# Kernel tuning notes

Measured on AMD Instinct MI355X. Metric: run time of the kernel, lower is better.

## Reference

```python
import jax, jax.numpy as jnp
import numpy as np
from jax import lax

B, D, H, W = 16, 256, 64, 64
P = 8  # patchsize
EPS = 1e-5


def setup_inputs() -> dict:
    key = jax.random.key(0)
    ks = jax.random.split(key, 8)
    s = 0.02
    return {
        "x": jax.random.normal(ks[0], (B, D, H, W), jnp.float32),
        "wq": jax.random.normal(ks[1], (D, D), jnp.float32) * s,
        "bq": jnp.zeros((D,), jnp.float32),
        "wk": jax.random.normal(ks[2], (D, D), jnp.float32) * s,
        "bk": jnp.zeros((D,), jnp.float32),
        "wv": jax.random.normal(ks[3], (D, D), jnp.float32) * s,
        "bv": jnp.zeros((D,), jnp.float32),
        "w_out": jax.random.normal(ks[4], (D, D, 3, 3), jnp.float32) * s,
        "b_out": jnp.zeros((D,), jnp.float32),
        "gamma": jnp.ones((D,), jnp.float32),
        "beta": jnp.zeros((D,), jnp.float32),
        "bn_mean": jnp.zeros((D,), jnp.float32),
        "bn_var": jnp.ones((D,), jnp.float32),
    }


def _conv1x1(x, w, b):
    # x: [b,c,h,w], w: [o,c] (1x1 conv) -> [b,o,h,w]
    return jnp.einsum('bchw,oc->bohw', x, w) + b[None, :, None, None]


def _to_patches(t, p):
    # [b,d,h,w] -> [b, p*p, d*hh*ww]  (matches view+permute(0,2,4,1,3,5)+view)
    b, d, h, w = t.shape
    hh, ww = h // p, w // p
    t = t.reshape(b, d, p, hh, p, ww).transpose(0, 2, 4, 1, 3, 5)
    return t.reshape(b, p * p, d * hh * ww)


def reference(x, wq, bq, wk, bk, wv, bv, w_out, b_out, gamma, beta, bn_mean, bn_var):
    b, d, h, w = x.shape
    p = P
    hh, ww = h // p, w // p

    q = _to_patches(_conv1x1(x, wq, bq), p)  # [b, p^2, d*hh*ww]
    k = _to_patches(_conv1x1(x, wk, bk), p)
    v = _to_patches(_conv1x1(x, wv, bv), p)

    scale = 1.0 / jnp.sqrt(jnp.asarray(q.shape[-1], q.dtype))
    scores = jnp.einsum('bqe,bke->bqk', q, k) * scale  # [b, p^2, p^2]
    attn = jax.nn.softmax(scores, axis=-1)
    out = jnp.einsum('bqk,bke->bqe', attn, v)  # [b, p^2, d*hh*ww]

    # [b,p,p,d,hh,ww] -> permute(0,3,1,4,2,5) -> [b,d,h,w]
    out = out.reshape(b, p, p, d, hh, ww).transpose(0, 3, 1, 4, 2, 5).reshape(b, d, h, w)

    # 3x3 conv, padding 1
    y = lax.conv_general_dilated(out, w_out, window_strides=(1, 1),
                                 padding=((1, 1), (1, 1)),
                                 dimension_numbers=('NCHW', 'OIHW', 'NCHW'))
    y = y + b_out[None, :, None, None]

    # BatchNorm2d (eval mode with running stats)
    inv = gamma / jnp.sqrt(bn_var + EPS)
    y = (y - bn_mean[None, :, None, None]) * inv[None, :, None, None] + beta[None, :, None, None]

    # LeakyReLU(0.2)
    return jnp.where(y >= 0, y, 0.2 * y)
```

## Files before the change

kernel.cpp:

```cpp
#include <hip/hip_runtime.h>
#include <hip/hip_bf16.h>

#define BB 16
#define SS 4096

typedef __attribute__((ext_vector_type(8))) short short8;
typedef __attribute__((ext_vector_type(4))) float float4v;

__global__ __launch_bounds__(256) void wprep_qkv(
    const float* __restrict__ wq, const float* __restrict__ wk,
    const float* __restrict__ wv, __hip_bfloat16* __restrict__ blob) {
  int chunk = blockIdx.x * 256 + threadIdx.x;
  int lane = chunk & 63;
  int ob = (chunk >> 6) & 15;
  int cb = (chunk >> 10) & 7;
  int which = chunk >> 13;
  const float* W = (which == 0) ? wq : (which == 1) ? wk : wv;
  int o = ob * 16 + (lane & 15);
  int c0 = cb * 32 + (lane >> 4) * 8;
  const float* p = W + o * 256 + c0;
  union { uint4 u; __hip_bfloat16 h[8]; } t;
#pragma unroll
  for (int j = 0; j < 8; ++j) t.h[j] = __float2bfloat16(p[j]);
  *reinterpret_cast<uint4*>(blob + (size_t)chunk * 8) = t.u;
}

__global__ __launch_bounds__(256) void qkv_mfma(
    const float* __restrict__ x, const __hip_bfloat16* __restrict__ blob,
    const float* __restrict__ bq, const float* __restrict__ bk,
    const float* __restrict__ bv,
    __hip_bfloat16* __restrict__ qb, __hip_bfloat16* __restrict__ kb,
    __hip_bfloat16* __restrict__ vb) {
  __shared__ short ls[64 * 40];
  const int which = blockIdx.z;
  const int b = blockIdx.y;
  const int s0 = blockIdx.x * 64;
  const float* bias = (which == 0) ? bq : (which == 1) ? bk : bv;
  __hip_bfloat16* outb = (which == 0) ? qb : kb;
  const int tid = threadIdx.x;
  const int wave = tid >> 6, lane = tid & 63;
  const int q = lane >> 4, m = lane & 15;
  const int sl = tid & 63;
  const int cg = tid >> 6;
  float4v acc[4][4] = {};

  for (int cb = 0; cb < 8; ++cb) {
    __syncthreads();
    {
      const float* xp = x + ((size_t)(b * 256 + cb * 32 + cg * 8)) * SS + s0 + sl;
      union { uint4 u; __hip_bfloat16 h[8]; } t;
#pragma unroll
      for (int i = 0; i < 8; ++i)
        t.h[i] = __float2bfloat16(xp[(size_t)i * SS]);
      *reinterpret_cast<uint4*>(&ls[sl * 40 + cg * 8]) = t.u;
    }
    __syncthreads();
    short8 af[4];
#pragma unroll
    for (int of = 0; of < 4; ++of)
      af[of] = *reinterpret_cast<const short8*>(
          blob +
          ((size_t)(((which * 8 + cb) * 16 + wave * 4 + of) * 64 + lane)) * 8);
    short8 xf[4];
#pragma unroll
    for (int sf = 0; sf < 4; ++sf)
      xf[sf] = *reinterpret_cast<const short8*>(&ls[(sf * 16 + m) * 40 + q * 8]);
#pragma unroll
    for (int of = 0; of < 4; ++of)
#pragma unroll
      for (int sf = 0; sf < 4; ++sf)
        acc[of][sf] = __builtin_amdgcn_mfma_f32_16x16x32_bf16(
            af[of], xf[sf], acc[of][sf], 0, 0, 0);
  }
  if (which == 2) {
    const int h = s0 >> 6;
#pragma unroll
    for (int of = 0; of < 4; ++of) {
      int o_base = wave * 64 + of * 16 + q * 4;
#pragma unroll
      for (int sf = 0; sf < 4; ++sf) {
        int w = sf * 16 + m;
        union { uint2 u; __hip_bfloat16 hh[4]; } t;
#pragma unroll
        for (int r = 0; r < 4; ++r)
          t.hh[r] = __float2bfloat16(acc[of][sf][r] + bias[o_base + r]);
        *reinterpret_cast<uint2*>(
            vb + ((size_t)((b * 64 + h) * 64 + w)) * 256 + o_base) = t.u;
      }
    }
  } else {
#pragma unroll
    for (int of = 0; of < 4; ++of) {
      int o_base = wave * 64 + of * 16 + q * 4;
#pragma unroll
      for (int r = 0; r < 4; ++r) {
        int o = o_base + r;
        float bi = bias[o];
        __hip_bfloat16* op = outb + ((size_t)(b * 256 + o)) * SS + s0 + m;
#pragma unroll
        for (int sf = 0; sf < 4; ++sf)
          op[sf * 16] = __float2bfloat16(acc[of][sf][r] + bi);
      }
    }
  }
}

__global__ __launch_bounds__(256) void scores_mfma(
    const __hip_bfloat16* __restrict__ qb, const __hip_bfloat16* __restrict__ kb,
    float* __restrict__ scores) {
  const int b = blockIdx.y;
  const int d0 = blockIdx.x * 16;
  const int tid = threadIdx.x;
  const int wave = tid >> 6, lane = tid & 63;
  const int q = lane >> 4, m = lane & 15;
  const int t = wave * 16 + m;
  const int arow = (t >> 3) * 8;
  const int acol = (t & 7) * 8;
  float4v acc[4] = {};

  for (int dd = 0; dd < 16; ++dd) {
    const int d = d0 + dd;
    const __hip_bfloat16* qp = qb + ((size_t)(b * 256 + d)) * SS;
    const __hip_bfloat16* kp = kb + ((size_t)(b * 256 + d)) * SS;
#pragma unroll
    for (int khalf = 0; khalf < 2; ++khalf) {
      const int oh = khalf * 4 + q;
      short8 af = *reinterpret_cast<const short8*>(
          qp + (arow + oh) * 64 + acol);
      short8 bf[4];
#pragma unroll
      for (int nt = 0; nt < 4; ++nt) {
        int tp = nt * 16 + m;
        bf[nt] = *reinterpret_cast<const short8*>(
            kp + ((tp >> 3) * 8 + oh) * 64 + (tp & 7) * 8);
      }
#pragma unroll
      for (int nt = 0; nt < 4; ++nt)
        acc[nt] = __builtin_amdgcn_mfma_f32_16x16x32_bf16(af, bf[nt], acc[nt],
                                                          0, 0, 0);
    }
  }
#pragma unroll
  for (int nt = 0; nt < 4; ++nt)
#pragma unroll
    for (int r = 0; r < 4; ++r)
      atomicAdd(&scores[(b * 64 + wave * 16 + q * 4 + r) * 64 + nt * 16 + m],
                acc[nt][r]);
}

__global__ __launch_bounds__(64) void softmax_kernel(
    const float* __restrict__ scores, __hip_bfloat16* __restrict__ attnb) {
  const int t = blockIdx.x;
  const int b = blockIdx.y;
  const int lane = threadIdx.x;
  float v = scores[(b * 64 + t) * 64 + lane] * 0.0078125f;
  float m = v;
#pragma unroll
  for (int off = 32; off >= 1; off >>= 1) m = fmaxf(m, __shfl_xor(m, off));
  float e = __expf(v - m);
  float s = e;
#pragma unroll
  for (int off = 32; off >= 1; off >>= 1) s += __shfl_xor(s, off);
  attnb[(b * 64 + t) * 64 + lane] = __float2bfloat16(e / s);
}

__global__ __launch_bounds__(256) void apply_mfma(
    const __hip_bfloat16* __restrict__ attnb, const __hip_bfloat16* __restrict__ vb,
    __hip_bfloat16* __restrict__ zb) {
  __shared__ short Vs[64][268];
  const int off = blockIdx.x;
  const int b = blockIdx.y;
  const int oh = off >> 3, ow = off & 7;
  const int tid = threadIdx.x;
#pragma unroll
  for (int i = 0; i < 8; ++i) {
    int chunk = i * 256 + tid;
    int tp = chunk >> 5;
    int cg = chunk & 31;
    int hh = (tp >> 3) * 8 + oh;
    int wwp = (tp & 7) * 8 + ow;
    uint4 val = *reinterpret_cast<const uint4*>(
        vb + ((size_t)((b * 64 + hh) * 64 + wwp)) * 256 + cg * 8);
    *reinterpret_cast<uint4*>(&Vs[tp][cg * 8]) = val;
  }
  __syncthreads();
  const int wave = tid >> 6, lane = tid & 63;
  const int q = lane >> 4, m = lane & 15;
  float4v acc[4][4] = {};
#pragma unroll
  for (int ks = 0; ks < 2; ++ks) {
    short8 af[4];
#pragma unroll
    for (int mt = 0; mt < 4; ++mt)
      af[mt] = *reinterpret_cast<const short8*>(
          attnb + (b * 64 + mt * 16 + m) * 64 + ks * 32 + q * 8);
    short8 bf[4];
#pragma unroll
    for (int nt = 0; nt < 4; ++nt) {
      int d = wave * 64 + nt * 16 + m;
      union { short8 v; short s[8]; } t;
#pragma unroll
      for (int j = 0; j < 8; ++j) t.s[j] = Vs[ks * 32 + q * 8 + j][d];
      bf[nt] = t.v;
    }
#pragma unroll
    for (int mt = 0; mt < 4; ++mt)
#pragma unroll
      for (int nt = 0; nt < 4; ++nt)
        acc[mt][nt] = __builtin_amdgcn_mfma_f32_16x16x32_bf16(
            af[mt], bf[nt], acc[mt][nt], 0, 0, 0);
  }
#pragma unroll
  for (int mt = 0; mt < 4; ++mt)
#pragma unroll
    for (int r = 0; r < 4; ++r) {
      int t = mt * 16 + q * 4 + r;
      int h = (t >> 3) * 8 + oh;
      int w = (t & 7) * 8 + ow;
      __hip_bfloat16* base = zb + ((size_t)((b * 64 + h) * 64 + w)) * 256;
#pragma unroll
      for (int nt = 0; nt < 4; ++nt)
        base[wave * 64 + nt * 16 + m] = __float2bfloat16(acc[mt][nt][r]);
    }
}

__global__ __launch_bounds__(256) void wprep(
    const float* __restrict__ wo, __hip_bfloat16* __restrict__ blob) {
  int chunk = blockIdx.x * 256 + threadIdx.x;
  int l = chunk & 63;
  int ob = (chunk >> 6) & 15;
  int cb = (chunk >> 10) & 7;
  int tap = chunk >> 13;
  int o = ob * 16 + (l & 15);
  int c0 = cb * 32 + (l >> 4) * 8;
  union { uint4 u; __hip_bfloat16 h[8]; } t;
#pragma unroll
  for (int j = 0; j < 8; ++j)
    t.h[j] = __float2bfloat16(wo[((size_t)(o * 256 + c0 + j)) * 9 + tap]);
  *reinterpret_cast<uint4*>(blob + (size_t)chunk * 8) = t.u;
}

__global__ __launch_bounds__(256) void conv_mfma(
    const __hip_bfloat16* __restrict__ z, const __hip_bfloat16* __restrict__ blob,
    const float* __restrict__ bo, const float* __restrict__ gm,
    const float* __restrict__ bt, const float* __restrict__ mn,
    const float* __restrict__ vr, float* __restrict__ out) {
  __shared__ short zs[2][3 * 66 * 40];
  const int idx0 = blockIdx.x;
  const int h = (idx0 & 7) * 8 + ((idx0 >> 3) & 7);
  const int b = idx0 >> 6;
  const int tid = threadIdx.x;
  const int wave = tid >> 6, lane = tid & 63;
  const int q = lane >> 4, m = lane & 15;
  float4v acc[4][4] = {};

  int s_r[4], s_wp[4], s_cg[4];
  bool s_ok[4];
  const __hip_bfloat16* s_base[4];
#pragma unroll
  for (int k = 0; k < 4; ++k) {
    int idx = tid + k * 256;
    bool act = idx < 792;
    int cg = idx & 3;
    int t2 = idx >> 2;
    int wpos = act ? (t2 % 66) : 0;
    int r = act ? (t2 / 66) : 0;
    int h_in = h - 1 + r;
    int w_in = wpos - 1;
    bool ok = act && h_in >= 0 && h_in < 64 && w_in >= 0 && w_in < 64;
    s_r[k] = r; s_wp[k] = wpos; s_cg[k] = cg; s_ok[k] = ok && act;
    s_ok[k] = ok;
    s_base[k] = z + ((size_t)((b * 64 + h_in) * 64 + w_in)) * 256 + cg * 8;
    if (!act) s_ok[k] = false;
    if (idx >= 792) { s_r[k] = 0; s_wp[k] = 0; s_cg[k] = 0; }
  }
  bool s_act[4];
#pragma unroll
  for (int k = 0; k < 4; ++k) s_act[k] = (tid + k * 256) < 792;

  uint4 pf[4];
#pragma unroll
  for (int k = 0; k < 4; ++k)
    pf[k] = s_ok[k] ? *reinterpret_cast<const uint4*>(s_base[k])
                    : make_uint4(0u, 0u, 0u, 0u);
#pragma unroll
  for (int k = 0; k < 4; ++k)
    if (s_act[k])
      *reinterpret_cast<uint4*>(
          &zs[0][(s_r[k] * 66 + s_wp[k]) * 40 + s_cg[k] * 8]) = pf[k];
  __syncthreads();

  for (int cb = 0; cb < 8; ++cb) {
    const short* cur = zs[cb & 1];
    short* nxt = zs[(cb + 1) & 1];
    if (cb < 7) {
#pragma unroll
      for (int k = 0; k < 4; ++k)
        pf[k] = s_ok[k] ? *reinterpret_cast<const uint4*>(
                              s_base[k] + (size_t)(cb + 1) * 32)
                        : make_uint4(0u, 0u, 0u, 0u);
    }
    for (int tap = 0; tap < 9; ++tap) {
      const int kh = tap / 3, kw = tap % 3;
      short8 wf[4];
#pragma unroll
      for (int of = 0; of < 4; ++of) {
        int ob = wave * 4 + of;
        wf[of] = *reinterpret_cast<const short8*>(
            blob + ((size_t)(((tap * 8 + cb) * 16 + ob) * 64 + lane)) * 8);
      }
      short8 zf[4];
#pragma unroll
      for (int wfi = 0; wfi < 4; ++wfi) {
        int wpos = wfi * 16 + m + kw;
        zf[wfi] = *reinterpret_cast<const short8*>(
            &cur[(kh * 66 + wpos) * 40 + q * 8]);
      }
#pragma unroll
      for (int of = 0; of < 4; ++of)
#pragma unroll
        for (int wfi = 0; wfi < 4; ++wfi)
          acc[of][wfi] = __builtin_amdgcn_mfma_f32_16x16x32_bf16(
              wf[of], zf[wfi], acc[of][wfi], 0, 0, 0);
    }
    if (cb < 7) {
#pragma unroll
      for (int k = 0; k < 4; ++k)
        if (s_act[k])
          *reinterpret_cast<uint4*>(
              &nxt[(s_r[k] * 66 + s_wp[k]) * 40 + s_cg[k] * 8]) = pf[k];
    }
    __syncthreads();
  }
#pragma unroll
  for (int of = 0; of < 4; ++of) {
    int o_base = wave * 64 + of * 16 + q * 4;
#pragma unroll
    for (int r = 0; r < 4; ++r) {
      int o = o_base + r;
      float sc = gm[o] * rsqrtf(vr[o] + 1e-5f);
      float sh = bt[o] + (bo[o] - mn[o]) * sc;
#pragma unroll
      for (int wfi = 0; wfi < 4; ++wfi) {
        float y = acc[of][wfi][r] * sc + sh;
        y = (y >= 0.f) ? y : 0.2f * y;
        out[(((size_t)(b * 256 + o)) * 64 + h) * 64 + wfi * 16 + m] = y;
      }
    }
  }
}

extern "C" void kernel_launch(void* const* d_in, const int* in_sizes, int n_in,
                              void* d_out, int out_size, void* d_ws,
                              size_t ws_size, hipStream_t stream) {
  (void)in_sizes; (void)n_in; (void)out_size; (void)ws_size;
  const float* x  = (const float*)d_in[0];
  const float* wq = (const float*)d_in[1];
  const float* bq = (const float*)d_in[2];
  const float* wk = (const float*)d_in[3];
  const float* bk = (const float*)d_in[4];
  const float* wv = (const float*)d_in[5];
  const float* bv = (const float*)d_in[6];
  const float* wo = (const float*)d_in[7];
  const float* bo = (const float*)d_in[8];
  const float* gm = (const float*)d_in[9];
  const float* bt = (const float*)d_in[10];
  const float* mn = (const float*)d_in[11];
  const float* vr = (const float*)d_in[12];
  float* out = (float*)d_out;

  char* ws = (char*)d_ws;
  __hip_bfloat16* qb = (__hip_bfloat16*)(ws);
  __hip_bfloat16* kb = (__hip_bfloat16*)(ws + 33554432);
  float* scores = (float*)(ws + 67108864);
  __hip_bfloat16* attnb = (__hip_bfloat16*)(ws + 67371008);
  __hip_bfloat16* blob = (__hip_bfloat16*)(ws + 67502080);
  __hip_bfloat16* vb = (__hip_bfloat16*)d_out;
  __hip_bfloat16* blob_a = (__hip_bfloat16*)((char*)d_out + 33554432);

  hipMemsetAsync(scores, 0, BB * 64 * 64 * sizeof(float), stream);
  wprep<<<288, 256, 0, stream>>>(wo, blob);
  wprep_qkv<<<96, 256, 0, stream>>>(wq, wk, wv, blob_a);
  qkv_mfma<<<dim3(64, BB, 3), 256, 0, stream>>>(x, blob_a, bq, bk, bv,
                                                qb, kb, vb);
  scores_mfma<<<dim3(16, BB), 256, 0, stream>>>(qb, kb, scores);
  softmax_kernel<<<dim3(64, BB), 64, 0, stream>>>(scores, attnb);
  apply_mfma<<<dim3(64, BB), 256, 0, stream>>>(attnb, vb, qb );
  conv_mfma<<<dim3(BB * 64), 256, 0, stream>>>(qb, blob, bo, gm, bt, mn, vr,
                                               out);
}
```

Before: 337.3 us.

## Compute two output rows per conv block to share the input halo

The 3x3 conv kernel now processes two adjacent output rows per block using 512 threads (8 waves split into 2 rows x 4 output-channel quarters), loading a 4-row halo tile into LDS instead of 3 rows per single output row. This cuts redundant input-row loads from global memory. Blocks are also remapped so that consecutive XCD-interleaved block IDs cover the same batch element. In exchange the LDS footprint per block grows, the grid halves, and each weight fragment is still loaded separately by both row-waves.

```diff
diff --git a/kernel.cpp b/kernel.cpp
--- a/kernel.cpp
+++ b/kernel.cpp
@@ -240,51 +240,51 @@
   *reinterpret_cast<uint4*>(blob + (size_t)chunk * 8) = t.u;
 }
 
-__global__ __launch_bounds__(256) void conv_mfma(
+__global__ __launch_bounds__(512, 4) void conv_mfma(
     const __hip_bfloat16* __restrict__ z, const __hip_bfloat16* __restrict__ blob,
     const float* __restrict__ bo, const float* __restrict__ gm,
     const float* __restrict__ bt, const float* __restrict__ mn,
     const float* __restrict__ vr, float* __restrict__ out) {
-  __shared__ short zs[2][3 * 66 * 40];
+  __shared__ short zs[2][4 * 66 * 40];
   const int idx0 = blockIdx.x;
-  const int h = (idx0 & 7) * 8 + ((idx0 >> 3) & 7);
-  const int b = idx0 >> 6;
+  const int xcd = idx0 & 7;
+  const int i = idx0 >> 3;
+  const int b = i & 15;
+  const int hp = xcd * 4 + (i >> 4);
   const int tid = threadIdx.x;
   const int wave = tid >> 6, lane = tid & 63;
   const int q = lane >> 4, m = lane & 15;
+  const int hrow = wave & 1;
+  const int oq = wave >> 1;
   float4v acc[4][4] = {};
 
-  int s_r[4], s_wp[4], s_cg[4];
-  bool s_ok[4];
-  const __hip_bfloat16* s_base[4];
-#pragma unroll
-  for (int k = 0; k < 4; ++k) {
-    int idx = tid + k * 256;
-    bool act = idx < 792;
+  int s_r[3], s_wp[3], s_cg[3];
+  bool s_ok[3], s_act[3];
+  const __hip_bfloat16* s_base[3];
+#pragma unroll
+  for (int k = 0; k < 3; ++k) {
+    int idx = tid + k * 512;
+    bool act = idx < 1056;
     int cg = idx & 3;
     int t2 = idx >> 2;
     int wpos = act ? (t2 % 66) : 0;
     int r = act ? (t2 / 66) : 0;
-    int h_in = h - 1 + r;
+    int h_in = hp * 2 - 1 + r;
     int w_in = wpos - 1;
     bool ok = act && h_in >= 0 && h_in < 64 && w_in >= 0 && w_in < 64;
-    s_r[k] = r; s_wp[k] = wpos; s_cg[k] = cg; s_ok[k] = ok && act;
-    s_ok[k] = ok;
+    if (!act) { r = 0; wpos = 0; cg = 0; }
+    s_r[k] = r; s_wp[k] = wpos; s_cg[k] = cg;
+    s_ok[k] = ok; s_act[k] = act;
     s_base[k] = z + ((size_t)((b * 64 + h_in) * 64 + w_in)) * 256 + cg * 8;
-    if (!act) s_ok[k] = false;
-    if (idx >= 792) { s_r[k] = 0; s_wp[k] = 0; s_cg[k] = 0; }
-  }
-  bool s_act[4];
-#pragma unroll
-  for (int k = 0; k < 4; ++k) s_act[k] = (tid + k * 256) < 792;
-
-  uint4 pf[4];
-#pragma unroll
-  for (int k = 0; k < 4; ++k)
+  }
+
+  uint4 pf[3];
+#pragma unroll
+  for (int k = 0; k < 3; ++k)
     pf[k] = s_ok[k] ? *reinterpret_cast<const uint4*>(s_base[k])
                     : make_uint4(0u, 0u, 0u, 0u);
 #pragma unroll
-  for (int k = 0; k < 4; ++k)
+  for (int k = 0; k < 3; ++k)
     if (s_act[k])
       *reinterpret_cast<uint4*>(
           &zs[0][(s_r[k] * 66 + s_wp[k]) * 40 + s_cg[k] * 8]) = pf[k];
@@ -295,7 +295,7 @@
     short* nxt = zs[(cb + 1) & 1];
     if (cb < 7) {
 #pragma unroll
-      for (int k = 0; k < 4; ++k)
+      for (int k = 0; k < 3; ++k)
         pf[k] = s_ok[k] ? *reinterpret_cast<const uint4*>(
                               s_base[k] + (size_t)(cb + 1) * 32)
                         : make_uint4(0u, 0u, 0u, 0u);
@@ -305,7 +305,7 @@
       short8 wf[4];
 #pragma unroll
       for (int of = 0; of < 4; ++of) {
-        int ob = wave * 4 + of;
+        int ob = oq * 4 + of;
         wf[of] = *reinterpret_cast<const short8*>(
             blob + ((size_t)(((tap * 8 + cb) * 16 + ob) * 64 + lane)) * 8);
       }
@@ -314,7 +314,7 @@
       for (int wfi = 0; wfi < 4; ++wfi) {
         int wpos = wfi * 16 + m + kw;
         zf[wfi] = *reinterpret_cast<const short8*>(
-            &cur[(kh * 66 + wpos) * 40 + q * 8]);
+            &cur[((hrow + kh) * 66 + wpos) * 40 + q * 8]);
       }
 #pragma unroll
       for (int of = 0; of < 4; ++of)
@@ -325,16 +325,17 @@
     }
     if (cb < 7) {
 #pragma unroll
-      for (int k = 0; k < 4; ++k)
+      for (int k = 0; k < 3; ++k)
         if (s_act[k])
           *reinterpret_cast<uint4*>(
               &nxt[(s_r[k] * 66 + s_wp[k]) * 40 + s_cg[k] * 8]) = pf[k];
     }
     __syncthreads();
   }
+  const int h_out = hp * 2 + hrow;
 #pragma unroll
   for (int of = 0; of < 4; ++of) {
-    int o_base = wave * 64 + of * 16 + q * 4;
+    int o_base = oq * 64 + of * 16 + q * 4;
 #pragma unroll
     for (int r = 0; r < 4; ++r) {
       int o = o_base + r;
@@ -344,7 +345,7 @@
       for (int wfi = 0; wfi < 4; ++wfi) {
         float y = acc[of][wfi][r] * sc + sh;
         y = (y >= 0.f) ? y : 0.2f * y;
-        out[(((size_t)(b * 256 + o)) * 64 + h) * 64 + wfi * 16 + m] = y;
+        out[(((size_t)(b * 256 + o)) * 64 + h_out) * 64 + wfi * 16 + m] = y;
       }
     }
   }
@@ -386,6 +387,6 @@
   scores_mfma<<<dim3(16, BB), 256, 0, stream>>>(qb, kb, scores);
   softmax_kernel<<<dim3(64, BB), 64, 0, stream>>>(scores, attnb);
   apply_mfma<<<dim3(64, BB), 256, 0, stream>>>(attnb, vb, qb );
-  conv_mfma<<<dim3(BB * 64), 256, 0, stream>>>(qb, blob, bo, gm, bt, mn, vr,
-                                               out);
-}
+  conv_mfma<<<dim3(512), 512, 0, stream>>>(qb, blob, bo, gm, bt, mn, vr,
+                                           out);
+}
```

New measurement: 420.5 us. +24.7%, slower.
